# Kernel optimization log

Measured on AMD Instinct MI355X. Metric: run time of the kernel, lower is better.

## Reference

```python
import jax, jax.numpy as jnp
from jax import lax
import numpy as np

VOCAB, EMBED, HID = 128, 256, 1024
BATCH, SEQ = 64, 1024


def setup_inputs() -> dict:
    key = jax.random.key(0)
    ks = jax.random.split(key, 8)
    s = 0.05  # small init scale so tanh/sigmoid gates are not saturated
    return {
        "ids": jax.random.randint(ks[0], (BATCH, SEQ), 0, VOCAB, dtype=jnp.int32),
        "emb": jax.random.normal(ks[1], (VOCAB, EMBED), jnp.float32) * s,
        "w_in": jax.random.normal(ks[2], (EMBED, 3 * HID), jnp.float32) * s,
        "b_in": jnp.zeros((3 * HID,), jnp.float32),
        "w_rec": jax.random.normal(ks[3], (HID, 3 * HID), jnp.float32) * s,
        "b_rec": jnp.zeros((3 * HID,), jnp.float32),
        "w_out": jax.random.normal(ks[4], (HID, VOCAB), jnp.float32) * s,
        "b_out": jnp.zeros((VOCAB,), jnp.float32),
    }


def reference(ids, emb, w_in, b_in, w_rec, b_rec, w_out, b_out):
    # Embedding lookup: [B,T,E]
    x = emb[ids]
    # Input-side gate pre-activations computed for all timesteps at once: [B,T,3H]
    xg = x @ w_in + b_in
    B = x.shape[0]
    H = w_rec.shape[0]
    h0 = jnp.zeros((B, H), x.dtype)  # gru.get_initial_state -> zeros

    def step(h, xg_t):
        # Keras GRU, reset_after=True: recurrent bias added BEFORE reset-gate product
        rg = h @ w_rec + b_rec                      # [B,3H]
        xz, xr, xh = jnp.split(xg_t, 3, axis=-1)
        rz, rr, rh = jnp.split(rg, 3, axis=-1)
        z = jax.nn.sigmoid(xz + rz)                 # update gate
        r = jax.nn.sigmoid(xr + rr)                 # reset gate
        hh = jnp.tanh(xh + r * rh)                  # candidate
        h_new = z * h + (1.0 - z) * hh
        return h_new, h_new

    _, hs = lax.scan(step, h0, jnp.swapaxes(xg, 0, 1))  # hs: [T,B,H]
    hs = jnp.swapaxes(hs, 0, 1)                          # [B,T,H]
    logits = hs @ w_out + b_out                          # [B,T,V]
    return logits
```

## Files before the change

kernel.cpp:

```cpp
#include <hip/hip_runtime.h>
#include <hip/hip_bf16.h>
#include <hip/hip_fp16.h>
#include <cstddef>


#define VOCABN 128
#define HIDN   1024
#define BN     64
#define TN     1024
#define C3N    3072
#define NREP   2
#define FREP   3
#define NGRU   256
#define NLOG   256

typedef _Float16 half8 __attribute__((ext_vector_type(8)));
typedef float    f32x4 __attribute__((ext_vector_type(4)));
typedef unsigned int u32x4 __attribute__((ext_vector_type(4)));
typedef unsigned int u32x2 __attribute__((ext_vector_type(2)));

__global__ __launch_bounds__(256, 1) void emb_gemm(
    const float* __restrict__ emb, const float* __restrict__ w_in,
    const float* __restrict__ b_in, _Float16* __restrict__ Mtab)
{
    __shared__ float se[16][256];
    const int tid = threadIdx.x;
    const int c   = blockIdx.x * 256 + tid;
    const int v0  = blockIdx.y * 16;
#pragma unroll
    for (int i = 0; i < 16; ++i) {
        int flat = i * 256 + tid;
        int r = flat >> 8, e = flat & 255;
        se[r][e] = emb[(v0 + r) * 256 + e];
    }
    __syncthreads();
    float acc[16];
#pragma unroll
    for (int r = 0; r < 16; ++r) acc[r] = 0.f;
    for (int e = 0; e < 256; ++e) {
        float w = w_in[(size_t)e * C3N + c];
#pragma unroll
        for (int r = 0; r < 16; ++r) acc[r] = fmaf(se[r][e], w, acc[r]);
    }
    float bc = b_in[c];
#pragma unroll
    for (int r = 0; r < 16; ++r)
        Mtab[(size_t)(v0 + r) * C3N + c] = (_Float16)(acc[r] + bc);
}

__global__ __launch_bounds__(256, 1) void fused_persist(
    const int* __restrict__ ids, const _Float16* __restrict__ Mtab_g,
    const float* __restrict__ w_rec, const float* __restrict__ b_rec,
    _Float16* __restrict__ comm,
    unsigned int* __restrict__ flags,
    _Float16* __restrict__ hs,
    const float* __restrict__ w_out, const float* __restrict__ b_out,
    float* __restrict__ out)
{
    __shared__ __align__(16) char smem[46080];
    _Float16* wh   = (_Float16*)smem;
    _Float16* mtab = (_Float16*)(smem + 32768);
    _Float16* sht  = (_Float16*)(smem + 45056);
    const half8* whp = (const half8*)wh;

    const int tid = threadIdx.x;

    if (blockIdx.x >= NGRU) {
        _Float16* sa = (_Float16*)smem;
        const int wk = blockIdx.x - NGRU;
        for (int i = 0; i < 16; ++i) {
            const int tile = wk + NLOG * i;
            const int m0   = tile * 16;
            const int tn   = tile >> 2;
            const int pl   = tile & 3;
            if (tid < 64) {
                const unsigned int* pollp =
                    flags + 2 * 4096 + (tid * 4 + pl) * 16;
                const unsigned int tv = (unsigned int)(tn + 1);
                while (true) {
                    unsigned int f;
                    asm volatile("global_load_dword %0, %1, off sc0 sc1\n\t"
                                 "s_waitcnt vmcnt(0)"
                                 : "=v"(f) : "v"(pollp) : "memory");
                    if (__all(f >= tv)) break;
                    __builtin_amdgcn_s_sleep(64);
                }
            }
            __syncthreads();
#pragma unroll
            for (int j = 0; j < 8; ++j) {
                int flat = j * 256 + tid;
                int r = flat >> 7, kc = flat & 127;
                const _Float16* p = hs + (size_t)(m0 + r) * HIDN + kc * 8;
                u32x4 hv;
                asm volatile("global_load_dwordx4 %0, %1, off sc0 sc1\n\t"
                             "s_waitcnt vmcnt(0)"
                             : "=v"(hv) : "v"(p) : "memory");
                *(u32x4*)(sa + (size_t)r * HIDN + kc * 8) = hv;
            }
            __syncthreads();
            const int v = tid & 127, g = tid >> 7;
            float acc[8];
#pragma unroll
            for (int r = 0; r < 8; ++r) acc[r] = 0.f;
            for (int k = 0; k < 1024; ++k) {
                float wv = w_out[(size_t)k * VOCABN + v];
#pragma unroll
                for (int r = 0; r < 8; ++r)
                    acc[r] = fmaf((float)sa[(size_t)(g * 8 + r) * HIDN + k],
                                  wv, acc[r]);
            }
            float bo = b_out[v];
#pragma unroll
            for (int r = 0; r < 8; ++r) {
                int m = m0 + g * 8 + r;
                out[((size_t)(m & 63) * TN + (m >> 6)) * VOCABN + v] = acc[r] + bo;
            }
            __syncthreads();
        }
        return;
    }

    if (tid >= 64) return;
    const int l  = tid;
    const int w  = blockIdx.x & 63;
    const int mt = blockIdx.x >> 6;
    const int jj = l & 15;
    const int lh = l >> 4;

    for (int i = 0; i < 256; ++i) {
        int flat = i * 64 + l;
        int e  = flat & 7;
        int ll = (flat >> 3) & 63;
        int kt = flat >> 9;
        int k   = kt * 32 + (ll >> 4) * 8 + e;
        int col = 2048 + w * 16 + (ll & 15);
        wh[(kt * 64 + ll) * 8 + e] = (_Float16)w_rec[(size_t)k * C3N + col];
    }
    for (int i = 0; i < 96; ++i) {
        int flat = i * 64 + l;
        int v = flat / 48, c = flat % 48;
        int col = (c >> 4) * 1024 + w * 16 + (c & 15);
        mtab[v * 48 + c] = Mtab_g[(size_t)v * C3N + col];
    }
    half8 wz[32], wr[32];
#pragma unroll
    for (int kt = 0; kt < 32; ++kt) {
#pragma unroll
        for (int e = 0; e < 8; ++e) {
            int k = kt * 32 + lh * 8 + e;
            wz[kt][e] = (_Float16)w_rec[(size_t)k * C3N + w * 16 + jj];
            wr[kt][e] = (_Float16)w_rec[(size_t)k * C3N + 1024 + w * 16 + jj];
        }
    }
    const float bz = b_rec[w * 16 + jj];
    const float br = b_rec[1024 + w * 16 + jj];
    const float bh = b_rec[2048 + w * 16 + jj];
    asm volatile("s_waitcnt lgkmcnt(0)" ::: "memory");
    __builtin_amdgcn_sched_barrier(0);

    const int bbase = mt * 16 + lh * 4;
    float hprev[4] = {0.f, 0.f, 0.f, 0.f};

    const int ktp = w >> 1;
    _Float16* cw_base = comm + (size_t)mt * 16384 + ktp * 512
                      + (w & 1) * 256 + l * 4;
    const _Float16* cr_base = comm + (size_t)(w & 1) * 131072
                            + (size_t)mt * 16384 + (size_t)l * 8;
    unsigned int* myflag = flags + (w * 4 + mt) * 16;
    const unsigned int* pollp = flags + (w & 1) * 4096 + (l * 4 + mt) * 16;

    const int Bq  = (l >> 1) & 15;
    const int jq  = 8 * (l >> 5) + (l & 1) * 4;
    _Float16* hs_base = hs + (size_t)(mt * 16 + Bq) * HIDN + w * 16 + jq;

    int idsv[4];
#pragma unroll
    for (int q = 0; q < 4; ++q) idsv[q] = ids[(size_t)(bbase + q) * TN];

#define ISSUE(BUF, G) do { _Pragma("unroll")                                  \
    for (int i_ = 0; i_ < 8; ++i_)                                            \
        asm volatile("global_load_dwordx4 %0, %1, off sc0 sc1"                \
            : "=v"(BUF[i_]) : "v"(crd + (8*(G)+i_) * 512) : "memory");        \
    } while (0)

#define WAITN(N) do {                                                         \
    asm volatile("s_waitcnt vmcnt(" #N ")" ::: "memory");                     \
    __builtin_amdgcn_sched_barrier(0); } while (0)

#define PROCG(BUF, G) do { _Pragma("unroll")                                  \
    for (int i_ = 0; i_ < 8; ++i_) {                                          \
        half8 a_ = __builtin_bit_cast(half8, BUF[i_]);                        \
        int kt_ = 8*(G) + i_;                                                 \
        acc0 = __builtin_amdgcn_mfma_f32_16x16x32_f16(a_, wz[kt_], acc0, 0, 0, 0); \
        acc1 = __builtin_amdgcn_mfma_f32_16x16x32_f16(a_, wr[kt_], acc1, 0, 0, 0); \
        acc2 = __builtin_amdgcn_mfma_f32_16x16x32_f16(a_, whp[kt_ * 64 + l], acc2, 0, 0, 0); \
    } } while (0)

    for (int t = 0; t < TN; ++t) {
        {
            const unsigned int tv = (unsigned int)t;
            while (true) {
                unsigned int f;
                asm volatile("global_load_dword %0, %1, off sc0 sc1\n\t"
                             "s_waitcnt vmcnt(0)"
                             : "=v"(f) : "v"(pollp) : "memory");
                if (__all(f >= tv)) break;
                __builtin_amdgcn_s_sleep(1);
            }
        }
        __builtin_amdgcn_sched_barrier(0);

        const _Float16* crd = cr_base + (size_t)(t & 1) * 65536;
        u32x4 bA[8], bB[8], bC[8];
        f32x4 acc0 = {0.f, 0.f, 0.f, 0.f};
        f32x4 acc1 = {0.f, 0.f, 0.f, 0.f};
        f32x4 acc2 = {0.f, 0.f, 0.f, 0.f};

        ISSUE(bA, 0); ISSUE(bB, 1); ISSUE(bC, 2);
        WAITN(16); PROCG(bA, 0); ISSUE(bA, 3);
        WAITN(16); PROCG(bB, 1);
        WAITN(8);  PROCG(bC, 2);
        WAITN(0);  PROCG(bA, 3);

        float hnv[4];
#pragma unroll
        for (int q = 0; q < 4; ++q) {
            float az = acc0[q], ar = acc1[q], ah = acc2[q];
            int id = idsv[q];
            float xz = (float)mtab[id * 48 + jj];
            float xr = (float)mtab[id * 48 + 16 + jj];
            float xh = (float)mtab[id * 48 + 32 + jj];
            float z  = 1.f / (1.f + __expf(-(xz + az + bz)));
            float r  = 1.f / (1.f + __expf(-(xr + ar + br)));
            float hh = tanhf(xh + r * (ah + bh));
            float hn = z * hprev[q] + (1.f - z) * hh;
            hprev[q] = hn;
            hnv[q] = hn;
        }
#pragma unroll
        for (int q = 0; q < 4; ++q)
            sht[(lh * 4 + q) * 16 + jj] = (_Float16)hnv[q];
        asm volatile("s_waitcnt lgkmcnt(0)" ::: "memory");
        __builtin_amdgcn_sched_barrier(0);
        {
            u32x2 pk = *(const u32x2*)&sht[Bq * 16 + jq];
            _Float16* hp = hs_base + (size_t)t * BN * HIDN;
            asm volatile("global_store_dwordx2 %0, %1, off sc0 sc1"
                         :: "v"(hp), "v"(pk) : "memory");
            _Float16* cwp = cw_base + (size_t)((t + 1) & 1) * 65536;
#pragma unroll
            for (int rr = 0; rr < NREP; ++rr)
                asm volatile("global_store_dwordx2 %0, %1, off sc0 sc1"
                             :: "v"(cwp + rr * 131072), "v"(pk) : "memory");
        }
        if (t + 1 < TN) {
#pragma unroll
            for (int q = 0; q < 4; ++q)
                idsv[q] = ids[(size_t)(bbase + q) * TN + t + 1];
            WAITN(4);
        } else {
            WAITN(0);
        }
        if (l == 0) {
            unsigned int fv = (unsigned int)(t + 1);
#pragma unroll
            for (int rr = 0; rr < FREP; ++rr)
                asm volatile("global_store_dword %0, %1, off sc0 sc1"
                             :: "v"(myflag + rr * 4096), "v"(fv) : "memory");
        }
    }
#undef ISSUE
#undef WAITN
#undef PROCG
}

extern "C" void kernel_launch(void* const* d_in, const int* in_sizes, int n_in,
                              void* d_out, int out_size, void* d_ws, size_t ws_size,
                              hipStream_t stream) {
    const int*   ids   = (const int*)d_in[0];
    const float* emb   = (const float*)d_in[1];
    const float* w_in  = (const float*)d_in[2];
    const float* b_in  = (const float*)d_in[3];
    const float* w_rec = (const float*)d_in[4];
    const float* b_rec = (const float*)d_in[5];
    const float* w_out = (const float*)d_in[6];
    const float* b_out = (const float*)d_in[7];
    float* out = (float*)d_out;

    char* ws = (char*)d_ws;
    _Float16* Mtab = (_Float16*)ws;
    size_t off = (size_t)VOCABN * C3N * 2;
    _Float16* comm = (_Float16*)(ws + off); off += (size_t)NREP * 131072 * 2;
    unsigned int* flags = (unsigned int*)(ws + off); off += FREP * 4096 * 4;
    _Float16* hs = (_Float16*)(ws + off);

    emb_gemm<<<dim3(12, 8), 256, 0, stream>>>(emb, w_in, b_in, Mtab);
    hipMemsetAsync(comm, 0, (size_t)NREP * 131072 * 2, stream);
    hipMemsetAsync(flags, 0, FREP * 4096 * 4, stream);

    fused_persist<<<NGRU + NLOG, 256, 0, stream>>>(
        ids, Mtab, w_rec, b_rec, comm, flags, hs, w_out, b_out, out);
}
```

Baseline: 4.654 ms.

## Use MFMA for output projection with pre-packed fp16 w_out and pipelined loads

Adds a prep kernel that converts w_out to fp16 in an MFMA fragment layout. The logits blocks now compute each 16-row tile with 16x16x32 f16 MFMAs instead of a scalar FMA loop over LDS. hs and weight fragments are loaded straight from global memory into registers with double-buffered software pipelining, which removes the LDS staging and the block barriers. All four waves poll the flags independently, and the poll sleep is shortened. The cost is a large register footprint per thread and fp16 precision for w_out.

```diff
diff --git a/kernel.cpp b/kernel.cpp
--- a/kernel.cpp
+++ b/kernel.cpp
@@ -48,14 +48,28 @@
         Mtab[(size_t)(v0 + r) * C3N + c] = (_Float16)(acc[r] + bc);
 }
 
+__global__ __launch_bounds__(64, 1) void wout_prep(
+    const float* __restrict__ w_out, _Float16* __restrict__ woutf)
+{
+    const int blk = blockIdx.x;
+    const int l   = threadIdx.x;
+    const int col   = ((blk >> 5) * 16) + (l & 15);
+    const int kbase = (blk & 31) * 32 + (l >> 4) * 8;
+    half8 v;
+#pragma unroll
+    for (int e = 0; e < 8; ++e)
+        v[e] = (_Float16)w_out[(size_t)(kbase + e) * VOCABN + col];
+    *(half8*)(woutf + ((size_t)blk * 64 + l) * 8) = v;
+}
+
 __global__ __launch_bounds__(256, 1) void fused_persist(
     const int* __restrict__ ids, const _Float16* __restrict__ Mtab_g,
     const float* __restrict__ w_rec, const float* __restrict__ b_rec,
     _Float16* __restrict__ comm,
     unsigned int* __restrict__ flags,
     _Float16* __restrict__ hs,
-    const float* __restrict__ w_out, const float* __restrict__ b_out,
-    float* __restrict__ out)
+    const _Float16* __restrict__ woutf,
+    const float* __restrict__ b_out, float* __restrict__ out)
 {
     __shared__ __align__(16) char smem[46080];
     _Float16* wh   = (_Float16*)smem;
@@ -66,16 +80,48 @@
     const int tid = threadIdx.x;
 
     if (blockIdx.x >= NGRU) {
-        _Float16* sa = (_Float16*)smem;
         const int wk = blockIdx.x - NGRU;
+        const int l  = tid & 63;
+        const int mw = tid >> 6;
+        const int jl = l & 15, hl = l >> 4;
+        const int ct0 = mw * 2, ct1 = mw * 2 + 1;
+        const float bo0 = b_out[ct0 * 16 + jl];
+        const float bo1 = b_out[ct1 * 16 + jl];
+        const _Float16* b0base = woutf + ((size_t)ct0 * 32 * 64 + l) * 8;
+        const _Float16* b1base = woutf + ((size_t)ct1 * 32 * 64 + l) * 8;
+
+#define LISS(BUF, P) do { _Pragma("unroll")                                   \
+    for (int k8 = 0; k8 < 8; ++k8) {                                          \
+        int kt_ = 8*(P) + k8;                                                 \
+        asm volatile("global_load_dwordx4 %0, %1, off sc0 sc1"                \
+            : "=v"(BUF[3*k8+0]) : "v"(abase + kt_*32) : "memory");            \
+        asm volatile("global_load_dwordx4 %0, %1, off"                        \
+            : "=v"(BUF[3*k8+1]) : "v"(b0base + kt_*512) : "memory");          \
+        asm volatile("global_load_dwordx4 %0, %1, off"                        \
+            : "=v"(BUF[3*k8+2]) : "v"(b1base + kt_*512) : "memory");          \
+    } } while (0)
+
+#define LWAIT(N) do {                                                         \
+    asm volatile("s_waitcnt vmcnt(" #N ")" ::: "memory");                     \
+    __builtin_amdgcn_sched_barrier(0); } while (0)
+
+#define LPROC(BUF) do { _Pragma("unroll")                                     \
+    for (int k8 = 0; k8 < 8; ++k8) {                                          \
+        half8 a_  = __builtin_bit_cast(half8, BUF[3*k8+0]);                   \
+        half8 b0_ = __builtin_bit_cast(half8, BUF[3*k8+1]);                   \
+        half8 b1_ = __builtin_bit_cast(half8, BUF[3*k8+2]);                   \
+        acc0 = __builtin_amdgcn_mfma_f32_16x16x32_f16(a_, b0_, acc0, 0, 0, 0);\
+        acc1 = __builtin_amdgcn_mfma_f32_16x16x32_f16(a_, b1_, acc1, 0, 0, 0);\
+    } } while (0)
+
         for (int i = 0; i < 16; ++i) {
             const int tile = wk + NLOG * i;
             const int m0   = tile * 16;
             const int tn   = tile >> 2;
             const int pl   = tile & 3;
-            if (tid < 64) {
+            {
                 const unsigned int* pollp =
-                    flags + 2 * 4096 + (tid * 4 + pl) * 16;
+                    flags + 2 * 4096 + (l * 4 + pl) * 16;
                 const unsigned int tv = (unsigned int)(tn + 1);
                 while (true) {
                     unsigned int f;
@@ -83,41 +129,30 @@
                                  "s_waitcnt vmcnt(0)"
                                  : "=v"(f) : "v"(pollp) : "memory");
                     if (__all(f >= tv)) break;
-                    __builtin_amdgcn_s_sleep(64);
+                    __builtin_amdgcn_s_sleep(32);
                 }
             }
-            __syncthreads();
-#pragma unroll
-            for (int j = 0; j < 8; ++j) {
-                int flat = j * 256 + tid;
-                int r = flat >> 7, kc = flat & 127;
-                const _Float16* p = hs + (size_t)(m0 + r) * HIDN + kc * 8;
-                u32x4 hv;
-                asm volatile("global_load_dwordx4 %0, %1, off sc0 sc1\n\t"
-                             "s_waitcnt vmcnt(0)"
-                             : "=v"(hv) : "v"(p) : "memory");
-                *(u32x4*)(sa + (size_t)r * HIDN + kc * 8) = hv;
+            __builtin_amdgcn_sched_barrier(0);
+            const _Float16* abase = hs + (size_t)(m0 + jl) * HIDN + hl * 8;
+            u32x4 PA[24], PB[24];
+            f32x4 acc0 = {0.f, 0.f, 0.f, 0.f};
+            f32x4 acc1 = {0.f, 0.f, 0.f, 0.f};
+            LISS(PA, 0); LISS(PB, 1);
+            LWAIT(24); LPROC(PA); LISS(PA, 2);
+            LWAIT(24); LPROC(PB); LISS(PB, 3);
+            LWAIT(24); LPROC(PA);
+            LWAIT(0);  LPROC(PB);
+#pragma unroll
+            for (int q = 0; q < 4; ++q) {
+                int m = m0 + hl * 4 + q;
+                size_t ro = ((size_t)(m & 63) * TN + (m >> 6)) * VOCABN;
+                out[ro + ct0 * 16 + jl] = acc0[q] + bo0;
+                out[ro + ct1 * 16 + jl] = acc1[q] + bo1;
             }
-            __syncthreads();
-            const int v = tid & 127, g = tid >> 7;
-            float acc[8];
-#pragma unroll
-            for (int r = 0; r < 8; ++r) acc[r] = 0.f;
-            for (int k = 0; k < 1024; ++k) {
-                float wv = w_out[(size_t)k * VOCABN + v];
-#pragma unroll
-                for (int r = 0; r < 8; ++r)
-                    acc[r] = fmaf((float)sa[(size_t)(g * 8 + r) * HIDN + k],
-                                  wv, acc[r]);
-            }
-            float bo = b_out[v];
-#pragma unroll
-            for (int r = 0; r < 8; ++r) {
-                int m = m0 + g * 8 + r;
-                out[((size_t)(m & 63) * TN + (m >> 6)) * VOCABN + v] = acc[r] + bo;
-            }
-            __syncthreads();
-        }
+        }
+#undef LISS
+#undef LWAIT
+#undef LPROC
         return;
     }
 
@@ -293,12 +328,14 @@
     size_t off = (size_t)VOCABN * C3N * 2;
     _Float16* comm = (_Float16*)(ws + off); off += (size_t)NREP * 131072 * 2;
     unsigned int* flags = (unsigned int*)(ws + off); off += FREP * 4096 * 4;
+    _Float16* woutf = (_Float16*)(ws + off); off += (size_t)HIDN * VOCABN * 2;
     _Float16* hs = (_Float16*)(ws + off);
 
     emb_gemm<<<dim3(12, 8), 256, 0, stream>>>(emb, w_in, b_in, Mtab);
+    wout_prep<<<256, 64, 0, stream>>>(w_out, woutf);
     hipMemsetAsync(comm, 0, (size_t)NREP * 131072 * 2, stream);
     hipMemsetAsync(flags, 0, FREP * 4096 * 4, stream);
 
     fused_persist<<<NGRU + NLOG, 256, 0, stream>>>(
-        ids, Mtab, w_rec, b_rec, comm, flags, hs, w_out, b_out, out);
+        ids, Mtab, w_rec, b_rec, comm, flags, hs, woutf, b_out, out);
 }
```

After: 3.857 ms (median of 2 runs). 1.21x faster.
